# Kernel tuning notes

Measured on AMD Instinct MI355X. Metric: run time of the kernel, lower is better.

Reference implementation:

```python
import jax, jax.numpy as jnp
import numpy as np

N, E = 20000, 320000
F_IN = 32
LAYERS = [32, 32, 32, 32]
NB = 4            # basis terms per spatial dim (dims=[4,4])
B = NB * NB       # tensor-product basis size
OUT_SCALE = 1.0 / 128.0


def _hat(x, n):
    # 'linear' RBF: hat functions with centers on linspace(-1,1,n)
    c = jnp.linspace(-1.0, 1.0, n, dtype=x.dtype)
    r = jnp.abs(x[:, None] - c[None, :]) * ((n - 1) * 0.5)
    return jnp.maximum(1.0 - r, 0.0)  # [E, n]


def _edge_basis(edge_attr, edge_i, edge_j):
    # cartesian coordinate mapping: clamp relative positions to [-1,1]
    d = jnp.clip(edge_attr, -1.0, 1.0)
    phi = (_hat(d[:, 0], NB)[:, :, None] * _hat(d[:, 1], NB)[:, None, :]).reshape(-1, B)
    # centerIgnore: zero contribution of self-edges (same math as filtering them)
    mask = (edge_i != edge_j).astype(phi.dtype)
    return phi * mask[:, None]  # [E, B]


def _basis_conv(x, W, phi, edge_i, edge_j, n_nodes):
    # continuous conv: gather sender feats, tensor-product with basis, GEMM, scatter-add
    x_j = x[edge_j]                                                      # [E, Fin]
    A = (phi[:, :, None] * x_j[:, None, :]).reshape(x_j.shape[0], -1)    # [E, B*Fin]
    msg = A @ W.reshape(-1, W.shape[-1])                                 # [E, Fout]
    return jnp.zeros((n_nodes, W.shape[-1]), x.dtype).at[edge_i].add(msg)


def setup_inputs() -> dict:
    key = jax.random.key(0)
    ks = jax.random.split(key, 6)
    fluidFeatures = jax.random.normal(ks[0], (N, F_IN), jnp.float32)
    edge_i = jax.random.randint(ks[1], (E,), 0, N)
    edge_j = jax.random.randint(ks[2], (E,), 0, N)
    edge_attr = jax.random.uniform(ks[3], (E, 2), jnp.float32, -1.0, 1.0)
    conv_ws, fc_ws, fc_bs = [], [], []
    in_f = F_IN
    for li, out_f in enumerate(LAYERS):
        kw = jax.random.fold_in(ks[4], li)
        conv_ws.append(jax.random.normal(kw, (B, in_f, out_f), jnp.float32) / np.sqrt(34.0 * B * in_f))
        kf = jax.random.fold_in(ks[5], li)
        fc_ws.append(jax.random.normal(kf, (in_f, out_f), jnp.float32) / np.sqrt(in_f))
        fc_bs.append(jnp.zeros((out_f,), jnp.float32))
        in_f = out_f
    return {"fluidFeatures": fluidFeatures, "edge_i": edge_i, "edge_j": edge_j,
            "edge_attr": edge_attr, "conv_ws": conv_ws, "fc_ws": fc_ws, "fc_bs": fc_bs}


def reference(fluidFeatures, edge_i, edge_j, edge_attr, conv_ws, fc_ws, fc_bs):
    n_nodes = fluidFeatures.shape[0]
    phi = _edge_basis(edge_attr, edge_i, edge_j)  # shared across layers
    ans = (_basis_conv(fluidFeatures, conv_ws[0], phi, edge_i, edge_j, n_nodes)
           + fluidFeatures @ fc_ws[0] + fc_bs[0])
    for l in range(1, len(conv_ws)):
        a = jax.nn.relu(ans)
        new = (_basis_conv(a, conv_ws[l], phi, edge_i, edge_j, n_nodes)
               + a @ fc_ws[l] + fc_bs[l])
        ans = new + ans if new.shape == ans.shape else new  # residual when widths match
    return ans * OUT_SCALE
```

## Files before the change

### kernel.cpp

```cpp
#include <hip/hip_runtime.h>
#include <hip/hip_bf16.h>

#define NN 20000
#define NE 320000
#define NCH 17
#define SROWU 552
#define CAP 64
#define W2U (2 * NCH * 512)

typedef __attribute__((ext_vector_type(8))) short short8;
typedef __attribute__((ext_vector_type(4))) float f32x4;

__device__ __forceinline__ unsigned short f2bf(float v) {
    unsigned u = __float_as_uint(v);
    unsigned r = (u + 0x7fffu + ((u >> 16) & 1u)) >> 16;
    return (unsigned short)r;
}
__device__ __forceinline__ float bf2f(unsigned short s) {
    return __uint_as_float(((unsigned)s) << 16);
}

struct WPtrs { const float* cw[4]; const float* fw[4]; };


__global__ __launch_bounds__(256) void buildfill_kernel(const int* __restrict__ ei,
                                                        const int* __restrict__ ej,
                                                        const float* __restrict__ attr,
                                                        int* __restrict__ cnt,
                                                        uint4* __restrict__ bucket,
                                                        WPtrs wp,
                                                        const float* __restrict__ feat,
                                                        unsigned* __restrict__ x0,
                                                        unsigned short* __restrict__ w2frag) {
    int b = blockIdx.x, t = threadIdx.x;
    if (b < 1250) {
        int e = b * 256 + t;
        int i = ei[e], j = ej[e];
        float2 a = ((const float2*)attr)[e];
        float d0 = fminf(fmaxf(a.x, -1.f), 1.f);
        float d1 = fminf(fmaxf(a.y, -1.f), 1.f);
        float tx = (d0 + 1.f) * 1.5f;
        float ty = (d1 + 1.f) * 1.5f;
        int ix = min(2, max(0, (int)floorf(tx)));
        int iy = min(2, max(0, (int)floorf(ty)));
        float ux = tx - (float)ix;
        float uy = ty - (float)iy;
        float m = (i != j) ? 1.f : 0.f;
        uint4 mm;
        mm.x = (unsigned)j | ((unsigned)(ix * 4 + iy) << 16);
        mm.y = (unsigned)f2bf((1.f - ux) * (1.f - uy) * m)
             | ((unsigned)f2bf((1.f - ux) * uy * m) << 16);
        mm.z = (unsigned)f2bf(ux * (1.f - uy) * m)
             | ((unsigned)f2bf(ux * uy * m) << 16);
        mm.w = 0;
        int slot = atomicAdd(&cnt[i], 1);
        if (slot < CAP) bucket[(size_t)i * CAP + slot] = mm;
    } else if (b < 1329) {
        int n = (b - 1250) * 256 + t;
        if (n < NN) {
            const float4* fr = (const float4*)(feat + (size_t)n * 32);
            float4 v0 = fr[0], v1 = fr[1], v2 = fr[2], v3 = fr[3];
            float4 v4 = fr[4], v5 = fr[5], v6 = fr[6], v7 = fr[7];
            float lo[16] = {v0.x, v0.y, v0.z, v0.w, v1.x, v1.y, v1.z, v1.w,
                            v2.x, v2.y, v2.z, v2.w, v3.x, v3.y, v3.z, v3.w};
            float hi[16] = {v4.x, v4.y, v4.z, v4.w, v5.x, v5.y, v5.z, v5.w,
                            v6.x, v6.y, v6.z, v6.w, v7.x, v7.y, v7.z, v7.w};
            unsigned o[16];
#pragma unroll
            for (int f = 0; f < 16; f++)
                o[f] = (unsigned)f2bf(lo[f]) | ((unsigned)f2bf(hi[f]) << 16);
            uint4* dst = (uint4*)(x0 + (size_t)n * 16);
#pragma unroll
            for (int q = 0; q < 4; q++) {
                uint4 w; w.x = o[q*4]; w.y = o[q*4+1]; w.z = o[q*4+2]; w.w = o[q*4+3];
                dst[q] = w;
            }
        }
    } else {
        int id2 = (b - 1329) * 256 + t;
        if (id2 < 8704) {
            int lane = id2 & 63;
            int c = (id2 >> 6) % NCH;
            int lt = id2 / (NCH * 64);
            int l = lt >> 1, tt = lt & 1;
            int kb = (lane >> 4) * 8;
            int col = tt * 16 + (lane & 15);
            short8 o;
#pragma unroll
            for (int i = 0; i < 8; i++) {
                int k = c * 32 + kb + i;
                float v = (k < 512) ? wp.cw[l][(size_t)k * 32 + col]
                                    : wp.fw[l][(size_t)(k - 512) * 32 + col];
                o[i] = (short)f2bf(v);
            }
            *(short8*)(w2frag + (size_t)id2 * 8) = o;
        }
    }
}

__global__ __launch_bounds__(1024, 8) void fused_kernel(const unsigned* __restrict__ xin,
                                                        unsigned short* __restrict__ xout,
                                                        const uint4* __restrict__ bucket,
                                                        const int* __restrict__ cnt,
                                                        const unsigned short* __restrict__ w2frag,
                                                        const float* __restrict__ bias,
                                                        float* __restrict__ ansbuf,
                                                        float* __restrict__ outf,
                                                        int mode) {
    __shared__ unsigned short su[16][SROWU];
    __shared__ __align__(16) float part[16][64][4];
    int tid = threadIdx.x;
    int wv = tid >> 6, lane = tid & 63;
    int fcol = lane & 15;
    int kg = lane >> 4;
    int node = blockIdx.x * 16 + wv;
    int deg = min(cnt[node], CAP);
    const uint4* em = bucket + (size_t)node * CAP;

    f32x4 acc0 = {0.f, 0.f, 0.f, 0.f};
    f32x4 acc1 = {0.f, 0.f, 0.f, 0.f};

    for (int qb = 0; qb < deg; qb += 32) {
        int last = deg - 1;
        int qa = qb + kg * 8;
        uint4 mm[8];
#pragma unroll
        for (int i = 0; i < 8; i++) mm[i] = em[min(qa + i, last)];
        unsigned xv[8];
#pragma unroll
        for (int i = 0; i < 8; i++)
            xv[i] = xin[(size_t)(mm[i].x & 0xFFFF) * 16 + fcol];
        short8 av, bv0, bv1;
#pragma unroll
        for (int i = 0; i < 8; i++) {
            bv0[i] = (short)(unsigned short)(xv[i] & 0xFFFF);
            bv1[i] = (short)(unsigned short)(xv[i] >> 16);
            int d = fcol - (int)(mm[i].x >> 16);
            unsigned bits = (d == 0) ? (mm[i].y & 0xFFFFu)
                          : (d == 1) ? (mm[i].y >> 16)
                          : (d == 4) ? (mm[i].z & 0xFFFFu)
                          : (d == 5) ? (mm[i].z >> 16) : 0u;
            if (qa + i >= deg) bits = 0u;
            av[i] = (short)bits;
        }
        acc0 = __builtin_amdgcn_mfma_f32_16x16x32_bf16(av, bv0, acc0, 0, 0, 0);
        acc1 = __builtin_amdgcn_mfma_f32_16x16x32_bf16(av, bv1, acc1, 0, 0, 0);
    }
#pragma unroll
    for (int r = 0; r < 4; r++) {
        int sr = kg * 4 + r;
        su[wv][sr * 32 + fcol]      = f2bf(acc0[r]);
        su[wv][sr * 32 + 16 + fcol] = f2bf(acc1[r]);
    }
    if (lane < 32) {
        unsigned xv = xin[(size_t)node * 16 + (lane & 15)];
        su[wv][512 + lane] = (unsigned short)((lane < 16) ? (xv & 0xFFFF) : (xv >> 16));
    }
    __syncthreads();

    {
        int tb = wv & 1;
        int s = wv >> 1;
        int row = lane & 15;
        int kb = (lane >> 4) * 8;
        const unsigned short* bp = w2frag + (size_t)tb * NCH * 512 + lane * 8;
        f32x4 acc = {0.f, 0.f, 0.f, 0.f};
#pragma unroll
        for (int k = 0; k < 3; k++) {
            int c = s + k * 8;
            if (c < NCH) {
                short8 av = *(const short8*)&su[row][c * 32 + kb];
                short8 bv = *(const short8*)(bp + (size_t)c * 512);
                acc = __builtin_amdgcn_mfma_f32_16x16x32_bf16(av, bv, acc, 0, 0, 0);
            }
        }
        *(f32x4*)&part[wv][lane][0] = acc;
    }
    __syncthreads();

    if (wv < 2) {
        f32x4 acc = *(const f32x4*)&part[wv][lane][0];
#pragma unroll
        for (int p = 1; p < 8; p++) {
            f32x4 q = *(const f32x4*)&part[wv + p * 2][lane][0];
            acc[0] += q[0]; acc[1] += q[1]; acc[2] += q[2]; acc[3] += q[3];
        }
        int fo = wv * 16 + (lane & 15);
        float bs = bias[fo];
        int xpos = (fo & 15) * 2 + (fo >> 4);
#pragma unroll
        for (int r = 0; r < 4; r++) {
            int nd = blockIdx.x * 16 + (lane >> 4) * 4 + r;
            float val = acc[r] + bs;
            if (mode) val += ansbuf[(size_t)nd * 32 + fo];
            if (mode == 2) {
                outf[(size_t)nd * 32 + fo] = val * (1.f / 128.f);
            } else {
                ansbuf[(size_t)nd * 32 + fo] = val;
                xout[(size_t)nd * 32 + xpos] = f2bf(fmaxf(val, 0.f));
            }
        }
    }
}

extern "C" void kernel_launch(void* const* d_in, const int* in_sizes, int n_in,
                              void* d_out, int out_size, void* d_ws, size_t ws_size,
                              hipStream_t stream) {
    const float* feat = (const float*)d_in[0];
    const int* ei = (const int*)d_in[1];
    const int* ej = (const int*)d_in[2];
    const float* attr = (const float*)d_in[3];
    WPtrs wp;
    const float* fcB[4];
    if (n_in >= 16) {
        for (int l = 0; l < 4; l++) {
            wp.cw[l] = (const float*)d_in[4 + l];
            wp.fw[l] = (const float*)d_in[8 + l];
            fcB[l]   = (const float*)d_in[12 + l];
        }
    } else {
        const float* cb = (const float*)d_in[4];
        const float* fb = (const float*)d_in[5];
        const float* bb = (const float*)d_in[6];
        for (int l = 0; l < 4; l++) {
            wp.cw[l] = cb + (size_t)l * 16 * 32 * 32;
            wp.fw[l] = fb + (size_t)l * 32 * 32;
            fcB[l]   = bb + (size_t)l * 32;
        }
    }

    char* p = (char*)d_ws;
    auto alloc = [&](size_t bytes) -> void* {
        void* r = (void*)p;
        p += (bytes + 255) & ~(size_t)255;
        return r;
    };
    unsigned short* w2frag = (unsigned short*)alloc((size_t)4 * W2U * sizeof(unsigned short));
    uint4* bucket = (uint4*)alloc((size_t)NN * CAP * sizeof(uint4));
    int* cnt      = (int*)alloc((size_t)NN * sizeof(int));
    unsigned* xA  = (unsigned*)alloc((size_t)NN * 16 * sizeof(unsigned));
    unsigned* xB  = (unsigned*)alloc((size_t)NN * 16 * sizeof(unsigned));
    float* ans    = (float*)alloc((size_t)NN * 32 * sizeof(float));
    float* outf   = (float*)d_out;

    hipMemsetAsync(cnt, 0, (size_t)NN * sizeof(int), stream);

    buildfill_kernel<<<1363, 256, 0, stream>>>(ei, ej, attr, cnt, bucket,
                                               wp, feat, xA, w2frag);

    fused_kernel<<<NN / 16, 1024, 0, stream>>>(xA, (unsigned short*)xB, bucket, cnt,
                                               w2frag + 0 * (size_t)W2U, fcB[0], ans, outf, 0);
    fused_kernel<<<NN / 16, 1024, 0, stream>>>(xB, (unsigned short*)xA, bucket, cnt,
                                               w2frag + 1 * (size_t)W2U, fcB[1], ans, outf, 1);
    fused_kernel<<<NN / 16, 1024, 0, stream>>>(xA, (unsigned short*)xB, bucket, cnt,
                                               w2frag + 2 * (size_t)W2U, fcB[2], ans, outf, 1);
    fused_kernel<<<NN / 16, 1024, 0, stream>>>(xB, (unsigned short*)xA, bucket, cnt,
                                               w2frag + 3 * (size_t)W2U, fcB[3], ans, outf, 2);
}
```

Measured before the change: 97.48 us.

## Run second-stage GEMM on two waves, drop partial-sum reduction, prefetch bias/residual

Measured after the change: 247.6 us. +154.0%, slower.

```diff
diff --git a/kernel.cpp b/kernel.cpp
--- a/kernel.cpp
+++ b/kernel.cpp
@@ -108,7 +108,6 @@
                                                         float* __restrict__ outf,
                                                         int mode) {
     __shared__ unsigned short su[16][SROWU];
-    __shared__ __align__(16) float part[16][64][4];
     int tid = threadIdx.x;
     int wv = tid >> 6, lane = tid & 63;
     int fcol = lane & 15;
@@ -117,30 +116,47 @@
     int deg = min(cnt[node], CAP);
     const uint4* em = bucket + (size_t)node * CAP;
 
+    float bsv = 0.f;
+    float resv[4] = {0.f, 0.f, 0.f, 0.f};
+    if (wv < 2) {
+        int fo = wv * 16 + (lane & 15);
+        bsv = bias[fo];
+        if (mode) {
+#pragma unroll
+            for (int r = 0; r < 4; r++)
+                resv[r] = ansbuf[(size_t)(blockIdx.x * 16 + (lane >> 4) * 4 + r) * 32 + fo];
+        }
+    }
+
     f32x4 acc0 = {0.f, 0.f, 0.f, 0.f};
     f32x4 acc1 = {0.f, 0.f, 0.f, 0.f};
 
     for (int qb = 0; qb < deg; qb += 32) {
-        int last = deg - 1;
         int qa = qb + kg * 8;
         uint4 mm[8];
-#pragma unroll
-        for (int i = 0; i < 8; i++) mm[i] = em[min(qa + i, last)];
         unsigned xv[8];
-#pragma unroll
-        for (int i = 0; i < 8; i++)
-            xv[i] = xin[(size_t)(mm[i].x & 0xFFFF) * 16 + fcol];
+        if (qa < deg) {
+            int last = deg - 1;
+#pragma unroll
+            for (int i = 0; i < 8; i++) mm[i] = em[min(qa + i, last)];
+#pragma unroll
+            for (int i = 0; i < 8; i++)
+                xv[i] = xin[(size_t)(mm[i].x & 0xFFFF) * 16 + fcol];
+        } else {
+#pragma unroll
+            for (int i = 0; i < 8; i++) {
+                mm[i].x = 0; mm[i].y = 0; mm[i].z = 0; mm[i].w = 0; xv[i] = 0;
+            }
+        }
         short8 av, bv0, bv1;
 #pragma unroll
         for (int i = 0; i < 8; i++) {
             bv0[i] = (short)(unsigned short)(xv[i] & 0xFFFF);
             bv1[i] = (short)(unsigned short)(xv[i] >> 16);
             int d = fcol - (int)(mm[i].x >> 16);
-            unsigned bits = (d == 0) ? (mm[i].y & 0xFFFFu)
-                          : (d == 1) ? (mm[i].y >> 16)
-                          : (d == 4) ? (mm[i].z & 0xFFFFu)
-                          : (d == 5) ? (mm[i].z >> 16) : 0u;
-            if (qa + i >= deg) bits = 0u;
+            unsigned sel = (d & 4) ? mm[i].z : mm[i].y;
+            unsigned bits = (d & 1) ? (sel >> 16) : (sel & 0xFFFFu);
+            if ((d & ~5) || (qa + i >= deg)) bits = 0u;
             av[i] = (short)bits;
         }
         acc0 = __builtin_amdgcn_mfma_f32_16x16x32_bf16(av, bv0, acc0, 0, 0, 0);
@@ -158,41 +174,23 @@
     }
     __syncthreads();
 
-    {
-        int tb = wv & 1;
-        int s = wv >> 1;
+    if (wv < 2) {
         int row = lane & 15;
         int kb = (lane >> 4) * 8;
-        const unsigned short* bp = w2frag + (size_t)tb * NCH * 512 + lane * 8;
+        const unsigned short* bp = w2frag + (size_t)wv * NCH * 512 + lane * 8;
         f32x4 acc = {0.f, 0.f, 0.f, 0.f};
 #pragma unroll
-        for (int k = 0; k < 3; k++) {
-            int c = s + k * 8;
-            if (c < NCH) {
-                short8 av = *(const short8*)&su[row][c * 32 + kb];
-                short8 bv = *(const short8*)(bp + (size_t)c * 512);
-                acc = __builtin_amdgcn_mfma_f32_16x16x32_bf16(av, bv, acc, 0, 0, 0);
-            }
-        }
-        *(f32x4*)&part[wv][lane][0] = acc;
-    }
-    __syncthreads();
-
-    if (wv < 2) {
-        f32x4 acc = *(const f32x4*)&part[wv][lane][0];
-#pragma unroll
-        for (int p = 1; p < 8; p++) {
-            f32x4 q = *(const f32x4*)&part[wv + p * 2][lane][0];
-            acc[0] += q[0]; acc[1] += q[1]; acc[2] += q[2]; acc[3] += q[3];
+        for (int c = 0; c < NCH; c++) {
+            short8 av = *(const short8*)&su[row][c * 32 + kb];
+            short8 bv = *(const short8*)(bp + (size_t)c * 512);
+            acc = __builtin_amdgcn_mfma_f32_16x16x32_bf16(av, bv, acc, 0, 0, 0);
         }
         int fo = wv * 16 + (lane & 15);
-        float bs = bias[fo];
         int xpos = (fo & 15) * 2 + (fo >> 4);
 #pragma unroll
         for (int r = 0; r < 4; r++) {
             int nd = blockIdx.x * 16 + (lane >> 4) * 4 + r;
-            float val = acc[r] + bs;
-            if (mode) val += ansbuf[(size_t)nd * 32 + fo];
+            float val = acc[r] + bsv + resv[r];
             if (mode == 2) {
                 outf[(size_t)nd * 32 + fo] = val * (1.f / 128.f);
             } else {
```
